# Optimization experiments

Hardware: AMD Instinct MI355X
Metric: run time of the kernel (lower is better)

Reference implementation:

```python
import jax, jax.numpy as jnp
import numpy as np

N = 50000      # nodes
D = 16         # regular in/out degree
E = N * D      # edges
IN_N = 128     # input node feature size
IN_E = 64      # input edge feature size
H = 64         # internal_size
H2 = 2 * H     # LSTM input/hidden size
OUT_N = 128
OUT_E = 64


def setup_inputs() -> dict:
    key = jax.random.key(0)
    ks = jax.random.split(key, 24)
    s = 0.05
    inp = {}
    inp["node_vecs"] = jax.random.normal(ks[0], (N, IN_N), jnp.float32)
    inp["edge_vecs"] = jax.random.normal(ks[1], (E, IN_E), jnp.float32)
    # ring digraph: edge e = i*D + k connects i -> (i+k+1) % N
    j = np.arange(N)[:, None]
    k = np.arange(D)[None, :]
    pni = (j - (k + 1)) % N
    inp["pred_node_idx"] = jnp.asarray(pni, jnp.int32)
    inp["pred_edge_idx"] = jnp.asarray(pni * D + k, jnp.int32)
    inp["succ_node_idx"] = jnp.asarray((j + k + 1) % N, jnp.int32)
    inp["succ_edge_idx"] = jnp.asarray(j * D + k, jnp.int32)
    src = np.repeat(np.arange(N), D)
    dst = (src + np.tile(np.arange(1, D + 1), N)) % N
    inp["edge_src"] = jnp.asarray(src, jnp.int32)
    inp["edge_dst"] = jnp.asarray(dst, jnp.int32)
    # parameters (torch Linear convention: y = x @ W.T + b)
    inp["Wn"] = jax.random.normal(ks[2], (H, IN_N), jnp.float32) * s
    inp["bn"] = jax.random.normal(ks[3], (H,), jnp.float32) * s
    inp["We"] = jax.random.normal(ks[4], (H, IN_E), jnp.float32) * s
    inp["be"] = jax.random.normal(ks[5], (H,), jnp.float32) * s
    # two LSTM aggregators (pred / succ), gate order i,f,g,o
    inp["Wih_p"] = jax.random.normal(ks[6], (4 * H2, H2), jnp.float32) * s
    inp["Whh_p"] = jax.random.normal(ks[7], (4 * H2, H2), jnp.float32) * s
    inp["bih_p"] = jax.random.normal(ks[8], (4 * H2,), jnp.float32) * s
    inp["bhh_p"] = jax.random.normal(ks[9], (4 * H2,), jnp.float32) * s
    inp["Wr_p"] = jax.random.normal(ks[10], (H, H2), jnp.float32) * s
    inp["br_p"] = jax.random.normal(ks[11], (H,), jnp.float32) * s
    inp["Wih_s"] = jax.random.normal(ks[12], (4 * H2, H2), jnp.float32) * s
    inp["Whh_s"] = jax.random.normal(ks[13], (4 * H2, H2), jnp.float32) * s
    inp["bih_s"] = jax.random.normal(ks[14], (4 * H2,), jnp.float32) * s
    inp["bhh_s"] = jax.random.normal(ks[15], (4 * H2,), jnp.float32) * s
    inp["Wr_s"] = jax.random.normal(ks[16], (H, H2), jnp.float32) * s
    inp["br_s"] = jax.random.normal(ks[17], (H,), jnp.float32) * s
    inp["Wt_n"] = jax.random.normal(ks[18], (OUT_N, 3 * H), jnp.float32) * s
    inp["bt_n"] = jax.random.normal(ks[19], (OUT_N,), jnp.float32) * s
    inp["Wt_e"] = jax.random.normal(ks[20], (OUT_E, 3 * H), jnp.float32) * s
    inp["bt_e"] = jax.random.normal(ks[21], (OUT_E,), jnp.float32) * s
    return inp


def _lstm_last(seq, Wih, Whh, bih, bhh):
    # seq: [N, D, 2H] -> last-timestep hidden state [N, 2H]
    n = seq.shape[0]
    h0 = jnp.zeros((n, H2), seq.dtype)

    def step(carry, x):
        h, c = carry
        g = x @ Wih.T + h @ Whh.T + (bih + bhh)
        i, f, gg, o = jnp.split(g, 4, axis=-1)
        c = jax.nn.sigmoid(f) * c + jax.nn.sigmoid(i) * jnp.tanh(gg)
        h = jax.nn.sigmoid(o) * jnp.tanh(c)
        return (h, c), None

    (h, _), _ = jax.lax.scan(step, (h0, h0), jnp.swapaxes(seq, 0, 1))
    return h


def _aggregate(hN, hE, nidx, eidx, Wih, Whh, bih, bhh, Wr, br):
    # gather neighbor sequences: concat(node pretrans, edge pretrans) -> [N, D, 2H]
    seq = jnp.concatenate([hN[nidx], hE[eidx]], axis=-1)
    h_last = _lstm_last(seq, Wih, Whh, bih, bhh)
    return jax.nn.relu(jax.nn.relu(h_last) @ Wr.T + br)  # [N, H]


def reference(node_vecs, edge_vecs, pred_node_idx, pred_edge_idx,
              succ_node_idx, succ_edge_idx, edge_src, edge_dst,
              Wn, bn, We, be,
              Wih_p, Whh_p, bih_p, bhh_p, Wr_p, br_p,
              Wih_s, Whh_s, bih_s, bhh_s, Wr_s, br_s,
              Wt_n, bt_n, Wt_e, bt_e):
    hN = jax.nn.relu(node_vecs @ Wn.T + bn)   # [N, H] node pretrans
    hE = jax.nn.relu(edge_vecs @ We.T + be)   # [E, H] edge pretrans
    agg_p = _aggregate(hN, hE, pred_node_idx, pred_edge_idx,
                       Wih_p, Whh_p, bih_p, bhh_p, Wr_p, br_p)
    agg_s = _aggregate(hN, hE, succ_node_idx, succ_edge_idx,
                       Wih_s, Whh_s, bih_s, bhh_s, Wr_s, br_s)
    node_in = jnp.concatenate([agg_p, hN, agg_s], axis=-1)      # [N, 3H]
    node_out = jax.nn.relu(node_in @ Wt_n.T + bt_n)             # [N, OUT_N]
    edge_in = jnp.concatenate([hN[edge_src], hE, hN[edge_dst]], axis=-1)  # [E, 3H]
    edge_out = jax.nn.relu(edge_in @ Wt_e.T + bt_e)             # [E, OUT_E]
    return node_out, edge_out
```

## Files before the change

### kernel.cpp

```cpp
#include <hip/hip_runtime.h>

#define DEV __device__ __forceinline__

typedef __bf16 bf16x8 __attribute__((ext_vector_type(8)));
typedef float floatx4 __attribute__((ext_vector_type(4)));
typedef unsigned short u16;

constexpr int NN    = 50000;
constexpr int DEG   = 16;
constexpr int H2    = 128;

constexpr size_t WS_WN    = 0;
constexpr size_t WS_WE    = 16384;
constexpr size_t WS_WIH_P = 24576;
constexpr size_t WS_WHH_P = 155648;
constexpr size_t WS_WR_P  = 286720;
constexpr size_t WS_WIH_S = 303104;
constexpr size_t WS_WHH_S = 434176;
constexpr size_t WS_WR_S  = 565248;
constexpr size_t WS_WT_N  = 581632;
constexpr size_t WS_WT_E  = 630784;
constexpr size_t WS_BSUM_P= 655360;
constexpr size_t WS_BSUM_S= 657408;
constexpr size_t WS_HN    = 659456;
constexpr size_t WS_AGGP  = 7059456;
constexpr size_t WS_AGGS  = 13459456;

DEV u16 f2bf(float x) {
  unsigned u = __builtin_bit_cast(unsigned, x);
  return (u16)((u + 0x7fffu + ((u >> 16) & 1u)) >> 16);
}
DEV bf16x8 ld8(const u16* p) { return *reinterpret_cast<const bf16x8*>(p); }
DEV floatx4 mfma16(bf16x8 a, bf16x8 b, floatx4 c) {
  return __builtin_amdgcn_mfma_f32_16x16x32_bf16(a, b, c, 0, 0, 0);
}
DEV floatx4 make4(float b) { floatx4 r = {b, b, b, b}; return r; }
DEV float sigf(float x) { return __builtin_amdgcn_rcpf(1.0f + __expf(-x)); }
DEV float tanh_(float x) {
  float e = __expf(-2.0f * fabsf(x));
  float r = (1.0f - e) * __builtin_amdgcn_rcpf(1.0f + e);
  return x >= 0.0f ? r : -r;
}
DEV bf16x8 relu8(bf16x8 a) {
  typedef u16 u16x8 __attribute__((ext_vector_type(8)));
  u16x8 u = __builtin_bit_cast(u16x8, a);
#pragma unroll
  for (int i = 0; i < 8; ++i) u[i] = (u[i] & 0x8000u) ? (u16)0 : u[i];
  return __builtin_bit_cast(bf16x8, u);
}

__global__ void k_prep(const float* Wn, const float* We,
                       const float* WihP, const float* WhhP, const float* WrP,
                       const float* WihS, const float* WhhS, const float* WrS,
                       const float* WtN, const float* WtE,
                       const float* bihP, const float* bhhP,
                       const float* bihS, const float* bhhS,
                       u16* wbf, float* bsumP, float* bsumS) {
  int idx = blockIdx.x * blockDim.x + threadIdx.x;
  if (idx < 327680) {
    const float* src; int rel;
    if      (idx <   8192) { src = Wn;   rel = idx; }
    else if (idx <  12288) { src = We;   rel = idx - 8192; }
    else if (idx <  77824) { src = WihP; rel = idx - 12288; }
    else if (idx < 143360) { src = WhhP; rel = idx - 77824; }
    else if (idx < 151552) { src = WrP;  rel = idx - 143360; }
    else if (idx < 217088) { src = WihS; rel = idx - 151552; }
    else if (idx < 282624) { src = WhhS; rel = idx - 217088; }
    else if (idx < 290816) { src = WrS;  rel = idx - 282624; }
    else if (idx < 315392) { src = WtN;  rel = idx - 290816; }
    else                   { src = WtE;  rel = idx - 315392; }
    wbf[idx] = f2bf(src[rel]);
  } else if (idx < 328704) {
    int j = idx - 327680;
    if (j < 512) bsumP[j] = bihP[j] + bhhP[j];
    else         bsumS[j - 512] = bihS[j - 512] + bhhS[j - 512];
  }
}

__global__ __launch_bounds__(256, 4) void k_pre_node(const float* xv, const float* bias,
                                                     const u16* Wbf, u16* outbf) {
  __shared__ __align__(16) u16 Xs[64 * 136];
  const int tid = threadIdx.x;
  const int base = blockIdx.x * 64;
#pragma unroll
  for (int j = 0; j < 8; ++j) {
    int flat = tid + j * 256;
    int row = flat >> 5, c4 = flat & 31;
    int gr = base + row; if (gr >= NN) gr = NN - 1;
    float4 v = reinterpret_cast<const float4*>(xv + (size_t)gr * 128)[c4];
    ushort4 h; h.x = f2bf(v.x); h.y = f2bf(v.y); h.z = f2bf(v.z); h.w = f2bf(v.w);
    *reinterpret_cast<ushort4*>(&Xs[row * 136 + c4 * 4]) = h;
  }
  __syncthreads();
  const int wave = tid >> 6, lane = tid & 63, l16 = lane & 15, quad = lane >> 4;
  const int rt = wave;
  floatx4 acc[4];
#pragma unroll
  for (int ct = 0; ct < 4; ++ct) acc[ct] = make4(bias[ct * 16 + l16]);
#pragma unroll
  for (int kt = 0; kt < 4; ++kt) {
    bf16x8 a = ld8(&Xs[(rt * 16 + l16) * 136 + kt * 32 + quad * 8]);
#pragma unroll
    for (int ct = 0; ct < 4; ++ct) {
      bf16x8 b = ld8(Wbf + (ct * 16 + l16) * 128 + kt * 32 + quad * 8);
      acc[ct] = mfma16(a, b, acc[ct]);
    }
  }
#pragma unroll
  for (int ct = 0; ct < 4; ++ct)
#pragma unroll
    for (int r = 0; r < 4; ++r) {
      int row = base + rt * 16 + quad * 4 + r;
      if (row < NN) {
        float v = acc[ct][r]; v = v > 0.0f ? v : 0.0f;
        outbf[(size_t)row * 64 + ct * 16 + l16] = f2bf(v);
      }
    }
}

__global__ __launch_bounds__(256, 4) void k_pre_edge(const float* xv, const float* bias,
                                                     const u16* Wbf, u16* outbf) {
  __shared__ __align__(16) u16 Xs[64 * 72];
  const int tid = threadIdx.x;
  const size_t base = (size_t)blockIdx.x * 64;
#pragma unroll
  for (int j = 0; j < 4; ++j) {
    int flat = tid + j * 256;
    int row = flat >> 4, c4 = flat & 15;
    float4 v = reinterpret_cast<const float4*>(xv + (base + row) * 64)[c4];
    ushort4 h; h.x = f2bf(v.x); h.y = f2bf(v.y); h.z = f2bf(v.z); h.w = f2bf(v.w);
    *reinterpret_cast<ushort4*>(&Xs[row * 72 + c4 * 4]) = h;
  }
  __syncthreads();
  const int wave = tid >> 6, lane = tid & 63, l16 = lane & 15, quad = lane >> 4;
  const int rt = wave;
  floatx4 acc[4];
#pragma unroll
  for (int ct = 0; ct < 4; ++ct) acc[ct] = make4(bias[ct * 16 + l16]);
#pragma unroll
  for (int kt = 0; kt < 2; ++kt) {
    bf16x8 a = ld8(&Xs[(rt * 16 + l16) * 72 + kt * 32 + quad * 8]);
#pragma unroll
    for (int ct = 0; ct < 4; ++ct) {
      bf16x8 b = ld8(Wbf + (ct * 16 + l16) * 64 + kt * 32 + quad * 8);
      acc[ct] = mfma16(a, b, acc[ct]);
    }
  }
#pragma unroll
  for (int ct = 0; ct < 4; ++ct)
#pragma unroll
    for (int r = 0; r < 4; ++r) {
      size_t row = base + rt * 16 + quad * 4 + r;
      float v = acc[ct][r]; v = v > 0.0f ? v : 0.0f;
      outbf[row * 128 + ct * 16 + l16] = f2bf(v);
    }
}

__global__ __launch_bounds__(512, 2) void k_lstm(
    const u16* hN, const u16* hE,
    const int* nidxP, const int* eidxP, const int* nidxS, const int* eidxS,
    const u16* WihP, const u16* WhhP, const float* bsumP, const u16* WrP, const float* brP, u16* aggP,
    const u16* WihS, const u16* WhhS, const float* bsumS, const u16* WrS, const float* brS, u16* aggS) {
  __shared__ __align__(16) u16 Xs[32 * 136];
  __shared__ __align__(16) u16 Hs[32 * 136];
  __shared__ int nidx_s[512], eidx_s[512];

  const bool s = (blockIdx.y != 0);
  const int* nidx = s ? nidxS : nidxP;
  const int* eidx = s ? eidxS : eidxP;
  const u16* Wih = s ? WihS : WihP;
  const u16* Whh = s ? WhhS : WhhP;
  const float* bsum = s ? bsumS : bsumP;
  const u16* Wr = s ? WrS : WrP;
  const float* br = s ? brS : brP;
  u16* aggOut = s ? aggS : aggP;

  const int tid = threadIdx.x;
  const int base = blockIdx.x * 32;
  {
    int g = base * 16 + tid;
    int vn = 0, ve = 0;
    if (g < NN * 16) { vn = nidx[g]; ve = eidx[g]; }
    nidx_s[tid] = vn; eidx_s[tid] = ve;
  }
  for (int j = tid; j < 32 * 136 / 2; j += 512) reinterpret_cast<unsigned*>(Hs)[j] = 0u;

  const int wave = tid >> 6, lane = tid & 63, l16 = lane & 15, quad = lane >> 4;

  bf16x8 wx[4][4], wh[4][4];
  float bias[4];
#pragma unroll
  for (int g = 0; g < 4; ++g) {
    int gc = g * 128 + wave * 16 + l16;
    bias[g] = bsum[gc];
#pragma unroll
    for (int kt = 0; kt < 4; ++kt) {
      wx[g][kt] = ld8(Wih + gc * 128 + kt * 32 + quad * 8);
      wh[g][kt] = ld8(Whh + gc * 128 + kt * 32 + quad * 8);
    }
  }
  floatx4 cst[2] = {make4(0.0f), make4(0.0f)};
  __syncthreads();

  const int srow = tid >> 4, sub = tid & 15, seg = sub >> 3, soff = (sub & 7) * 8;
  const u16* sbase = seg ? hE : hN;
  const size_t sstride = seg ? 128 : 64;
  const int* sidx = seg ? eidx_s : nidx_s;

  {
    int r0 = sidx[srow * 16];
    uint4 v0 = *reinterpret_cast<const uint4*>(sbase + (size_t)r0 * sstride + soff);
    *reinterpret_cast<uint4*>(&Xs[srow * 136 + seg * 64 + soff]) = v0;
  }
  __syncthreads();

  for (int t = 0; t < DEG; ++t) {
    int tn = (t + 1 < DEG) ? (t + 1) : t;
    int rn = sidx[srow * 16 + tn];
    uint4 vnext = *reinterpret_cast<const uint4*>(sbase + (size_t)rn * sstride + soff);

    floatx4 acc[4][2];
#pragma unroll
    for (int g = 0; g < 4; ++g) { acc[g][0] = make4(bias[g]); acc[g][1] = make4(bias[g]); }
#pragma unroll
    for (int kt = 0; kt < 4; ++kt) {
      bf16x8 a0 = ld8(&Xs[l16 * 136 + kt * 32 + quad * 8]);
      bf16x8 a1 = ld8(&Xs[(16 + l16) * 136 + kt * 32 + quad * 8]);
#pragma unroll
      for (int g = 0; g < 4; ++g) {
        acc[g][0] = mfma16(a0, wx[g][kt], acc[g][0]);
        acc[g][1] = mfma16(a1, wx[g][kt], acc[g][1]);
      }
    }
#pragma unroll
    for (int kt = 0; kt < 4; ++kt) {
      bf16x8 a0 = ld8(&Hs[l16 * 136 + kt * 32 + quad * 8]);
      bf16x8 a1 = ld8(&Hs[(16 + l16) * 136 + kt * 32 + quad * 8]);
#pragma unroll
      for (int g = 0; g < 4; ++g) {
        acc[g][0] = mfma16(a0, wh[g][kt], acc[g][0]);
        acc[g][1] = mfma16(a1, wh[g][kt], acc[g][1]);
      }
    }
    __syncthreads();

#pragma unroll
    for (int rtt = 0; rtt < 2; ++rtt) {
#pragma unroll
      for (int rr = 0; rr < 4; ++rr) {
        float gi = acc[0][rtt][rr], gf = acc[1][rtt][rr];
        float gg = acc[2][rtt][rr], go = acc[3][rtt][rr];
        float c = sigf(gf) * cst[rtt][rr] + sigf(gi) * tanh_(gg);
        float h = sigf(go) * tanh_(c);
        cst[rtt][rr] = c;
        Hs[(rtt * 16 + quad * 4 + rr) * 136 + wave * 16 + l16] = f2bf(h);
      }
    }

    if (t + 1 < DEG)
      *reinterpret_cast<uint4*>(&Xs[srow * 136 + seg * 64 + soff]) = vnext;
    __syncthreads();
  }

  {
    const int rt = wave >> 2, ct = wave & 3;
    floatx4 acc = make4(br[ct * 16 + l16]);
#pragma unroll
    for (int kt = 0; kt < 4; ++kt) {
      bf16x8 a = relu8(ld8(&Hs[(rt * 16 + l16) * 136 + kt * 32 + quad * 8]));
      bf16x8 b = ld8(Wr + (ct * 16 + l16) * 128 + kt * 32 + quad * 8);
      acc = mfma16(a, b, acc);
    }
#pragma unroll
    for (int rr = 0; rr < 4; ++rr) {
      int row = base + rt * 16 + quad * 4 + rr;
      if (row < NN) {
        float v = acc[rr] > 0.0f ? acc[rr] : 0.0f;
        aggOut[(size_t)row * 64 + ct * 16 + l16] = f2bf(v);
      }
    }
  }
}

__global__ __launch_bounds__(256, 4) void k_node_out(
    const u16* aggP, const u16* hN, const u16* aggS,
    const u16* Wt, const float* bt, float* outp) {
  __shared__ __align__(16) u16 Xs[64 * 200];
  const int tid = threadIdx.x;
  const int base = blockIdx.x * 64;
  const u16* segp[3] = {aggP, hN, aggS};
#pragma unroll
  for (int seg = 0; seg < 3; ++seg)
#pragma unroll
    for (int j = 0; j < 2; ++j) {
      int flat = tid + j * 256;
      int row = flat >> 3, off = (flat & 7) * 8;
      int gr = base + row; if (gr >= NN) gr = NN - 1;
      uint4 v = *reinterpret_cast<const uint4*>(segp[seg] + (size_t)gr * 64 + off);
      *reinterpret_cast<uint4*>(&Xs[row * 200 + seg * 64 + off]) = v;
    }
  __syncthreads();
  const int wave = tid >> 6, lane = tid & 63, l16 = lane & 15, quad = lane >> 4;
  const int rt = wave;
  floatx4 acc[8];
#pragma unroll
  for (int ct = 0; ct < 8; ++ct) acc[ct] = make4(bt[ct * 16 + l16]);
#pragma unroll
  for (int kt = 0; kt < 6; ++kt) {
    bf16x8 a = ld8(&Xs[(rt * 16 + l16) * 200 + kt * 32 + quad * 8]);
#pragma unroll
    for (int ct = 0; ct < 8; ++ct) {
      bf16x8 b = ld8(Wt + (ct * 16 + l16) * 192 + kt * 32 + quad * 8);
      acc[ct] = mfma16(a, b, acc[ct]);
    }
  }
#pragma unroll
  for (int ct = 0; ct < 8; ++ct)
#pragma unroll
    for (int r = 0; r < 4; ++r) {
      int row = base + rt * 16 + quad * 4 + r;
      if (row < NN) {
        float v = acc[ct][r];
        outp[(size_t)row * 128 + ct * 16 + l16] = v > 0.0f ? v : 0.0f;
      }
    }
}

__global__ __launch_bounds__(256, 4) void k_edge_out(
    const u16* hN, const u16* hE, const int* esrc, const int* edst,
    const u16* Wt, const float* bt, float* outp) {
  __shared__ __align__(16) u16 Xs[64 * 200];
  __shared__ int idxs[128];
  const int tid = threadIdx.x;
  const size_t base = (size_t)blockIdx.x * 64;
  if (tid < 64) idxs[tid] = esrc[base + tid];
  else if (tid < 128) idxs[tid] = edst[base + tid - 64];
  __syncthreads();
#pragma unroll
  for (int seg = 0; seg < 3; ++seg)
#pragma unroll
    for (int j = 0; j < 2; ++j) {
      int flat = tid + j * 256;
      int row = flat >> 3, off = (flat & 7) * 8;
      size_t grow;
      const u16* sp;
      if (seg == 0)      { grow = (size_t)idxs[row] * 64;       sp = hN; }
      else if (seg == 1) { grow = (base + row) * 128;           sp = hE; }
      else               { grow = (size_t)idxs[64 + row] * 64;  sp = hN; }
      uint4 v = *reinterpret_cast<const uint4*>(sp + grow + off);
      *reinterpret_cast<uint4*>(&Xs[row * 200 + seg * 64 + off]) = v;
    }
  __syncthreads();
  const int wave = tid >> 6, lane = tid & 63, l16 = lane & 15, quad = lane >> 4;
  const int rt = wave;
  floatx4 acc[4];
#pragma unroll
  for (int ct = 0; ct < 4; ++ct) acc[ct] = make4(bt[ct * 16 + l16]);
#pragma unroll
  for (int kt = 0; kt < 6; ++kt) {
    bf16x8 a = ld8(&Xs[(rt * 16 + l16) * 200 + kt * 32 + quad * 8]);
#pragma unroll
    for (int ct = 0; ct < 4; ++ct) {
      bf16x8 b = ld8(Wt + (ct * 16 + l16) * 192 + kt * 32 + quad * 8);
      acc[ct] = mfma16(a, b, acc[ct]);
    }
  }
#pragma unroll
  for (int ct = 0; ct < 4; ++ct)
#pragma unroll
    for (int r = 0; r < 4; ++r) {
      size_t row = base + rt * 16 + quad * 4 + r;
      float v = acc[ct][r];
      outp[row * 64 + ct * 16 + l16] = v > 0.0f ? v : 0.0f;
    }
}

extern "C" void kernel_launch(void* const* d_in, const int* in_sizes, int n_in,
                              void* d_out, int out_size, void* d_ws, size_t ws_size,
                              hipStream_t stream) {
  (void)in_sizes; (void)n_in; (void)out_size; (void)ws_size;
  const float* node_vecs = (const float*)d_in[0];
  const float* edge_vecs = (const float*)d_in[1];
  const int* pred_node_idx = (const int*)d_in[2];
  const int* pred_edge_idx = (const int*)d_in[3];
  const int* succ_node_idx = (const int*)d_in[4];
  const int* succ_edge_idx = (const int*)d_in[5];
  const int* edge_src = (const int*)d_in[6];
  const int* edge_dst = (const int*)d_in[7];
  const float* Wn = (const float*)d_in[8];
  const float* bn = (const float*)d_in[9];
  const float* We = (const float*)d_in[10];
  const float* be = (const float*)d_in[11];
  const float* Wih_p = (const float*)d_in[12];
  const float* Whh_p = (const float*)d_in[13];
  const float* bih_p = (const float*)d_in[14];
  const float* bhh_p = (const float*)d_in[15];
  const float* Wr_p = (const float*)d_in[16];
  const float* br_p = (const float*)d_in[17];
  const float* Wih_s = (const float*)d_in[18];
  const float* Whh_s = (const float*)d_in[19];
  const float* bih_s = (const float*)d_in[20];
  const float* bhh_s = (const float*)d_in[21];
  const float* Wr_s = (const float*)d_in[22];
  const float* br_s = (const float*)d_in[23];
  const float* Wt_n = (const float*)d_in[24];
  const float* bt_n = (const float*)d_in[25];
  const float* Wt_e = (const float*)d_in[26];
  const float* bt_e = (const float*)d_in[27];

  char* ws = (char*)d_ws;
  u16* wWn   = (u16*)(ws + WS_WN);
  u16* wWe   = (u16*)(ws + WS_WE);
  u16* wWihP = (u16*)(ws + WS_WIH_P);
  u16* wWhhP = (u16*)(ws + WS_WHH_P);
  u16* wWrP  = (u16*)(ws + WS_WR_P);
  u16* wWihS = (u16*)(ws + WS_WIH_S);
  u16* wWhhS = (u16*)(ws + WS_WHH_S);
  u16* wWrS  = (u16*)(ws + WS_WR_S);
  u16* wWtN  = (u16*)(ws + WS_WT_N);
  u16* wWtE  = (u16*)(ws + WS_WT_E);
  float* bsumP = (float*)(ws + WS_BSUM_P);
  float* bsumS = (float*)(ws + WS_BSUM_S);
  u16* hN   = (u16*)(ws + WS_HN);
  u16* aggP = (u16*)(ws + WS_AGGP);
  u16* aggS = (u16*)(ws + WS_AGGS);
  float* outN = (float*)d_out;
  float* outE = outN + (size_t)NN * 128;
  u16* hE = (u16*)outE;

  k_prep<<<1284, 256, 0, stream>>>(Wn, We, Wih_p, Whh_p, Wr_p, Wih_s, Whh_s, Wr_s,
                                   Wt_n, Wt_e, bih_p, bhh_p, bih_s, bhh_s,
                                   (u16*)ws, bsumP, bsumS);
  k_pre_node<<<782, 256, 0, stream>>>(node_vecs, bn, wWn, hN);
  k_pre_edge<<<12500, 256, 0, stream>>>(edge_vecs, be, wWe, hE);
  dim3 g3(1563, 2, 1);
  k_lstm<<<g3, 512, 0, stream>>>(hN, hE,
                                 pred_node_idx, pred_edge_idx, succ_node_idx, succ_edge_idx,
                                 wWihP, wWhhP, bsumP, wWrP, br_p, aggP,
                                 wWihS, wWhhS, bsumS, wWrS, br_s, aggS);
  k_node_out<<<782, 256, 0, stream>>>(aggP, hN, aggS, wWtN, bt_n, outN);
  k_edge_out<<<12500, 256, 0, stream>>>(hN, hE, edge_src, edge_dst, wWtE, bt_e, outE);
}
```

Baseline: 1.198 ms.

## Double-buffer LSTM X/H shared tiles to drop a barrier per timestep

The LSTM recurrence now ping-pongs the X and H tiles in shared memory, so each timestep reads the current buffer and writes the next one. That removes one of the two __syncthreads per step. The MFMA chains are reordered so the two row tiles are processed in sequence. The tanh is simplified to a branchless 2*sigmoid(2x)-1 form, which may overflow to inf for large negative inputs but still returns -1. The doubled shared memory use may reduce occupancy. After 16 steps the final H sits in buffer 0, which the output projection reads.

```diff
diff --git a/kernel.cpp b/kernel.cpp
--- a/kernel.cpp
+++ b/kernel.cpp
@@ -36,10 +36,9 @@
 }
 DEV floatx4 make4(float b) { floatx4 r = {b, b, b, b}; return r; }
 DEV float sigf(float x) { return __builtin_amdgcn_rcpf(1.0f + __expf(-x)); }
-DEV float tanh_(float x) {
-  float e = __expf(-2.0f * fabsf(x));
-  float r = (1.0f - e) * __builtin_amdgcn_rcpf(1.0f + e);
-  return x >= 0.0f ? r : -r;
+DEV float tanhb(float x) {
+  float e = __expf(-2.0f * x);
+  return __builtin_fmaf(2.0f, __builtin_amdgcn_rcpf(1.0f + e), -1.0f);
 }
 DEV bf16x8 relu8(bf16x8 a) {
   typedef u16 u16x8 __attribute__((ext_vector_type(8)));
@@ -161,8 +160,8 @@
     const int* nidxP, const int* eidxP, const int* nidxS, const int* eidxS,
     const u16* WihP, const u16* WhhP, const float* bsumP, const u16* WrP, const float* brP, u16* aggP,
     const u16* WihS, const u16* WhhS, const float* bsumS, const u16* WrS, const float* brS, u16* aggS) {
-  __shared__ __align__(16) u16 Xs[32 * 136];
-  __shared__ __align__(16) u16 Hs[32 * 136];
+  __shared__ __align__(16) u16 Xs[2][32 * 136];
+  __shared__ __align__(16) u16 Hs[2][32 * 136];
   __shared__ int nidx_s[512], eidx_s[512];
 
   const bool s = (blockIdx.y != 0);
@@ -183,7 +182,7 @@
     if (g < NN * 16) { vn = nidx[g]; ve = eidx[g]; }
     nidx_s[tid] = vn; eidx_s[tid] = ve;
   }
-  for (int j = tid; j < 32 * 136 / 2; j += 512) reinterpret_cast<unsigned*>(Hs)[j] = 0u;
+  for (int j = tid; j < 32 * 136 / 2; j += 512) reinterpret_cast<unsigned*>(Hs[0])[j] = 0u;
 
   const int wave = tid >> 6, lane = tid & 63, l16 = lane & 15, quad = lane >> 4;
 
@@ -210,11 +209,12 @@
   {
     int r0 = sidx[srow * 16];
     uint4 v0 = *reinterpret_cast<const uint4*>(sbase + (size_t)r0 * sstride + soff);
-    *reinterpret_cast<uint4*>(&Xs[srow * 136 + seg * 64 + soff]) = v0;
+    *reinterpret_cast<uint4*>(&Xs[0][srow * 136 + seg * 64 + soff]) = v0;
   }
   __syncthreads();
 
   for (int t = 0; t < DEG; ++t) {
+    const int cur = t & 1, nxt = cur ^ 1;
     int tn = (t + 1 < DEG) ? (t + 1) : t;
     int rn = sidx[srow * 16 + tn];
     uint4 vnext = *reinterpret_cast<const uint4*>(sbase + (size_t)rn * sstride + soff);
@@ -224,41 +224,44 @@
     for (int g = 0; g < 4; ++g) { acc[g][0] = make4(bias[g]); acc[g][1] = make4(bias[g]); }
 #pragma unroll
     for (int kt = 0; kt < 4; ++kt) {
-      bf16x8 a0 = ld8(&Xs[l16 * 136 + kt * 32 + quad * 8]);
-      bf16x8 a1 = ld8(&Xs[(16 + l16) * 136 + kt * 32 + quad * 8]);
-#pragma unroll
-      for (int g = 0; g < 4; ++g) {
-        acc[g][0] = mfma16(a0, wx[g][kt], acc[g][0]);
-        acc[g][1] = mfma16(a1, wx[g][kt], acc[g][1]);
+      bf16x8 a0 = ld8(&Xs[cur][l16 * 136 + kt * 32 + quad * 8]);
+#pragma unroll
+      for (int g = 0; g < 4; ++g) acc[g][0] = mfma16(a0, wx[g][kt], acc[g][0]);
+    }
+#pragma unroll
+    for (int kt = 0; kt < 4; ++kt) {
+      bf16x8 h0 = ld8(&Hs[cur][l16 * 136 + kt * 32 + quad * 8]);
+#pragma unroll
+      for (int g = 0; g < 4; ++g) acc[g][0] = mfma16(h0, wh[g][kt], acc[g][0]);
+    }
+#pragma unroll
+    for (int kt = 0; kt < 4; ++kt) {
+      bf16x8 a1 = ld8(&Xs[cur][(16 + l16) * 136 + kt * 32 + quad * 8]);
+#pragma unroll
+      for (int g = 0; g < 4; ++g) acc[g][1] = mfma16(a1, wx[g][kt], acc[g][1]);
+    }
+#pragma unroll
+    for (int kt = 0; kt < 4; ++kt) {
+      bf16x8 h1 = ld8(&Hs[cur][(16 + l16) * 136 + kt * 32 + quad * 8]);
+#pragma unroll
+      for (int g = 0; g < 4; ++g) acc[g][1] = mfma16(h1, wh[g][kt], acc[g][1]);
+    }
+
+#pragma unroll
+    for (int hh = 0; hh < 2; ++hh) {
+#pragma unroll
+      for (int rr = 0; rr < 4; ++rr) {
+        float gi = acc[0][hh][rr], gf = acc[1][hh][rr];
+        float gg = acc[2][hh][rr], go = acc[3][hh][rr];
+        float c = sigf(gf) * cst[hh][rr] + sigf(gi) * tanhb(gg);
+        float hv = sigf(go) * tanhb(c);
+        cst[hh][rr] = c;
+        Hs[nxt][(hh * 16 + quad * 4 + rr) * 136 + wave * 16 + l16] = f2bf(hv);
       }
     }
-#pragma unroll
-    for (int kt = 0; kt < 4; ++kt) {
-      bf16x8 a0 = ld8(&Hs[l16 * 136 + kt * 32 + quad * 8]);
-      bf16x8 a1 = ld8(&Hs[(16 + l16) * 136 + kt * 32 + quad * 8]);
-#pragma unroll
-      for (int g = 0; g < 4; ++g) {
-        acc[g][0] = mfma16(a0, wh[g][kt], acc[g][0]);
-        acc[g][1] = mfma16(a1, wh[g][kt], acc[g][1]);
-      }
-    }
-    __syncthreads();
-
-#pragma unroll
-    for (int rtt = 0; rtt < 2; ++rtt) {
-#pragma unroll
-      for (int rr = 0; rr < 4; ++rr) {
-        float gi = acc[0][rtt][rr], gf = acc[1][rtt][rr];
-        float gg = acc[2][rtt][rr], go = acc[3][rtt][rr];
-        float c = sigf(gf) * cst[rtt][rr] + sigf(gi) * tanh_(gg);
-        float h = sigf(go) * tanh_(c);
-        cst[rtt][rr] = c;
-        Hs[(rtt * 16 + quad * 4 + rr) * 136 + wave * 16 + l16] = f2bf(h);
-      }
-    }
 
     if (t + 1 < DEG)
-      *reinterpret_cast<uint4*>(&Xs[srow * 136 + seg * 64 + soff]) = vnext;
+      *reinterpret_cast<uint4*>(&Xs[nxt][srow * 136 + seg * 64 + soff]) = vnext;
     __syncthreads();
   }
 
@@ -267,7 +270,7 @@
     floatx4 acc = make4(br[ct * 16 + l16]);
 #pragma unroll
     for (int kt = 0; kt < 4; ++kt) {
-      bf16x8 a = relu8(ld8(&Hs[(rt * 16 + l16) * 136 + kt * 32 + quad * 8]));
+      bf16x8 a = relu8(ld8(&Hs[0][(rt * 16 + l16) * 136 + kt * 32 + quad * 8]));
       bf16x8 b = ld8(Wr + (ct * 16 + l16) * 128 + kt * 32 + quad * 8);
       acc = mfma16(a, b, acc);
     }
```

Result: faster. 1.147 ms (-4.3%).
